# Kernel tuning notes

Measured on AMD Instinct MI355X. Metric: run time of the kernel, lower is better.

The kernel has to match this reference:

```python
import jax, jax.numpy as jnp
import numpy as np

ALPHA = 0.2      # LeakyReLU negative slope (alpha)
KNN = 5          # knn_num / cluster_num in get_center_1
M = 5            # m in get_dc
CC = 3           # cluster_centers
NEG = -9e15
EPS = 9e-15

def _pdist(x):
    sq = jnp.sum(x * x, axis=1)
    d2 = sq[:, None] + sq[None, :] - 2.0 * (x @ x.T)
    return jnp.sqrt(jnp.maximum(d2, 0.0))

def _cdist(x, c):
    d2 = jnp.sum(x * x, 1)[:, None] + jnp.sum(c * c, 1)[None, :] - 2.0 * (x @ c.T)
    return jnp.sqrt(jnp.maximum(d2, 0.0))

def _kmeans(x, k=CC, iters=10):
    # deterministic stand-in for sklearn KMeans(n_clusters=3, init='k-means++'):
    # farthest-point init + fixed Lloyd iterations
    c0 = x[0]
    d = jnp.sum((x - c0) ** 2, 1)
    c1 = x[jnp.argmax(d)]
    d = jnp.minimum(d, jnp.sum((x - c1) ** 2, 1))
    c2 = x[jnp.argmax(d)]
    centers = jnp.stack([c0, c1, c2])
    def step(c, _):
        assign = jnp.argmin(_cdist(x, c), axis=1)
        oh = jax.nn.one_hot(assign, k, dtype=x.dtype)
        newc = (oh.T @ x) / jnp.maximum(oh.sum(0), 1.0)[:, None]
        return newc, None
    centers, _ = jax.lax.scan(step, centers, None, length=iters)
    return centers

def _gravity(h):
    # get_center_1: fully built from detached tensors in the original -> stop_gradient
    x = jax.lax.stop_gradient(h)
    n = x.shape[0]
    z = _pdist(x)                                 # [n, n] pairwise distances
    negv, loc = jax.lax.top_k(-z, M + 1)          # M+1 smallest distances per row
    dc = jnp.mean(-negv[:, 1])                    # mean nearest-neighbor distance
    knn_idx = loc[:, 1:KNN + 1]                   # 5-NN (excluding self)
    rows = jnp.arange(n)[:, None]
    knn_vals = jnp.take_along_axis(z, knn_idx, axis=1)
    ori = jnp.zeros_like(z).at[rows, knn_idx].set(knn_vals)   # dists only at 5-NN
    nearest = jnp.take_along_axis(ori, loc[:, 1:2], axis=1)
    safe = jnp.where(ori != 0, ori, 1.0)
    ori = jnp.where(ori != 0, dc * nearest / (safe * safe), ori)
    # replicate the source's global flat-index mask (index = arange(size).reshape)
    flat = jnp.arange(n * n).reshape(n, n)
    mincol = jnp.min(jnp.argsort(ori, axis=1)[:, -KNN:], axis=1, keepdims=True)
    ori = jnp.where(flat >= mincol, 0.0, ori) - EPS
    centers = _kmeans(x)
    d1 = _cdist(x, centers)                       # [n, 3] node->center distances
    nearest1 = d1[:, 1:2]                         # cupy wrap: (i*3+1) % 3 == 1
    safe1 = jnp.where(d1 != 0, d1, 1.0)
    d1 = jnp.where(d1 != 0, dc * nearest1 / (safe1 * safe1), d1) - EPS
    z3 = jnp.full((CC, CC), NEG, dtype=x.dtype)
    top = jnp.concatenate([ori, d1], axis=1)
    bot = jnp.concatenate([d1.T, z3], axis=1)
    return jnp.concatenate([top, bot], axis=0)    # [(n+3), (n+3)]

def _forward(h, W, a, t1, t2):
    n, fin = h.shape
    fout = W.shape[1]
    Wh = h @ W
    s = Wh @ a[:fout] + (Wh @ a[fout:]).T         # [n, n]
    e = jnp.where(s > 0, s, ALPHA * s)            # LeakyReLU attention logits
    g = _gravity(h)
    att = jnp.concatenate([
        jnp.concatenate([e, t1], axis=1),
        jnp.concatenate([t2, jnp.zeros((CC, CC), h.dtype)], axis=1),
    ], axis=0)                                    # [(n+3), (n+3)]
    att = jax.nn.softmax(g @ att, axis=1)         # dropout omitted (eval mode)
    h_pad = jnp.concatenate([h, jnp.zeros((CC, fin), h.dtype)], axis=0)
    out = att @ (h_pad @ W)                       # [(n+3), fout]
    return jax.nn.elu(out)                        # concat=True

def setup_inputs():
    key = jax.random.key(0)
    k = jax.random.split(key, 5)
    N, FIN, FOUT = 4096, 512, 64
    gain = 1.414
    limW = gain * np.sqrt(6.0 / (FIN + FOUT))
    lima = gain * np.sqrt(6.0 / (2 * FOUT + 1))
    return {
        "h": jax.random.normal(k[0], (N, FIN), jnp.float32),
        "adj": jnp.zeros((N, N), jnp.float32),   # accepted but unused by forward
        "W": jax.random.uniform(k[1], (FIN, FOUT), jnp.float32, -limW, limW),
        "a": jax.random.uniform(k[2], (2 * FOUT, 1), jnp.float32, -lima, lima),
        "t1": jax.random.normal(k[3], (N, CC), jnp.float32),
        "t2": jax.random.normal(k[4], (CC, N), jnp.float32),
    }

def reference(h, adj, W, a, t1, t2):
    return _forward(h, W, a, t1, t2)
```

## Files before the change

kernel.cpp:

```cpp
#include <hip/hip_runtime.h>
#include <hip/hip_bf16.h>
#include <math.h>

#define NPTS 4096
#define FIN 512
#define FOUT 64
#define SCALE 4194304.0f
#define INVSCALE 2.384185791015625e-7f

typedef __attribute__((ext_vector_type(8))) short bf16x8;
typedef __attribute__((ext_vector_type(4))) float f32x4;
typedef unsigned long long ull;

static __device__ __forceinline__ unsigned short bfbits(float x) {
  __hip_bfloat16 b = __float2bfloat16(x);
  return *reinterpret_cast<unsigned short*>(&b);
}

static __device__ __forceinline__ float wsum64(float v) {
  #pragma unroll
  for (int mm = 1; mm < 64; mm <<= 1) v += __shfl_xor(v, mm);
  return v;
}

static __device__ __forceinline__ int aloadi(int* p) {
  return __hip_atomic_load(p, __ATOMIC_RELAXED, __HIP_MEMORY_SCOPE_AGENT);
}
static __device__ __forceinline__ ull aloadu(ull* p) {
  return __hip_atomic_load(p, __ATOMIC_RELAXED, __HIP_MEMORY_SCOPE_AGENT);
}

__global__ __launch_bounds__(256) void k_prep(const float* __restrict__ h,
    const float* __restrict__ W, __hip_bfloat16* __restrict__ xb,
    float* __restrict__ sq, int* __restrict__ m1, __hip_bfloat16* __restrict__ WbT,
    ull* __restrict__ accZ, int* __restrict__ cntZ, int* __restrict__ barZ) {
  int bid = blockIdx.x, t = threadIdx.x;
  if (bid >= 1026) {
    int idx = (bid - 1026) * 256 + t;
    #pragma unroll
    for (int s = 0; s < 10; ++s) accZ[s * 1536 + idx] = 0ull;
    if (idx < 40) cntZ[idx] = 0;
    if (idx < 16) barZ[idx] = 0;
    return;
  }
  if (bid >= 1024) {
    int base = (bid - 1024) * 16384;
    for (int rep = 0; rep < 64; ++rep) {
      int e = base + rep * 256 + t;
      int n = e >> 9, k = e & 511;
      WbT[e] = __float2bfloat16(W[k * FOUT + n]);
    }
    return;
  }
  int lane = t & 63, wid = t >> 6;
  int row = bid * 4 + wid;
  const float4* hr = (const float4*)(h + (size_t)row * FIN);
  float4 a = hr[lane], b = hr[64 + lane];
  ushort4 pa = { bfbits(a.x), bfbits(a.y), bfbits(a.z), bfbits(a.w) };
  ushort4 pb = { bfbits(b.x), bfbits(b.y), bfbits(b.z), bfbits(b.w) };
  *(ushort4*)(xb + (size_t)row * FIN + 4 * lane) = pa;
  *(ushort4*)(xb + (size_t)row * FIN + 256 + 4 * lane) = pb;
  float s = a.x*a.x + a.y*a.y + a.z*a.z + a.w*a.w
          + b.x*b.x + b.y*b.y + b.z*b.z + b.w*b.w;
  s = wsum64(s);
  if (lane == 0) { sq[row] = s; m1[row] = 0x7F800000; }
}

__device__ __forceinline__ void gram_role(const __hip_bfloat16* __restrict__ xb,
    const float* __restrict__ sq, int* __restrict__ m1, int gb, char* smem) {
  bool act = threadIdx.x < 256;
  int tid = threadIdx.x;
  int lane = tid & 63, wid = tid >> 6;
  int b = gb, I = 0;
  while (b >= 32 - I) { b -= 32 - I; ++I; }
  int J = I + b;
  char* As = smem;
  char* Bs = smem + 16384;

  int R0 = I * 128, C0 = J * 128;
  int rowBase = (wid >> 1) * 64;
  int colBase = (wid & 1) * 64;
  int lrow = lane & 15, hi = lane >> 4, rsub = hi * 4;

  f32x4 acc[4][4];
  #pragma unroll
  for (int p = 0; p < 4; ++p)
    #pragma unroll
    for (int q = 0; q < 4; ++q)
      acc[p][q] = (f32x4){0.f, 0.f, 0.f, 0.f};

  int srow = lane >> 3;
  int scol = ((lane & 7) ^ srow) * 8;
  const __hip_bfloat16* gA = xb + (size_t)(R0 + (wid & 3) * 32 + srow) * FIN + scol;
  const __hip_bfloat16* gB = xb + (size_t)(C0 + (wid & 3) * 32 + srow) * FIN + scol;
  char* lA = As + (wid & 3) * 4096;
  char* lB = Bs + (wid & 3) * 4096;
  int rdswz = (lrow & 7) << 4;

  for (int kt = 0; kt < 8; ++kt) {
    int K0 = kt * 64;
    if (act) {
      #pragma unroll
      for (int j = 0; j < 4; ++j) {
        __builtin_amdgcn_global_load_lds(
            (const __attribute__((address_space(1))) unsigned int*)(gA + (size_t)(8 * j) * FIN + K0),
            (__attribute__((address_space(3))) unsigned int*)(lA + j * 1024), 16, 0, 0);
        __builtin_amdgcn_global_load_lds(
            (const __attribute__((address_space(1))) unsigned int*)(gB + (size_t)(8 * j) * FIN + K0),
            (__attribute__((address_space(3))) unsigned int*)(lB + j * 1024), 16, 0, 0);
      }
    }
    __syncthreads();
    if (act) {
      #pragma unroll
      for (int s = 0; s < 2; ++s) {
        int k0b = s * 64;
        bf16x8 av[4], bw[4];
        #pragma unroll
        for (int f = 0; f < 4; ++f) {
          int arow = rowBase + f * 16 + lrow;
          av[f] = *(const bf16x8*)(As + arow * 128 + ((k0b + hi * 16) ^ rdswz));
          int brow = colBase + f * 16 + lrow;
          bw[f] = *(const bf16x8*)(Bs + brow * 128 + ((k0b + hi * 16) ^ rdswz));
        }
        #pragma unroll
        for (int fi = 0; fi < 4; ++fi)
          #pragma unroll
          for (int fj = 0; fj < 4; ++fj)
            acc[fi][fj] = __builtin_amdgcn_mfma_f32_16x16x32_bf16(av[fi], bw[fj], acc[fi][fj], 0, 0, 0);
      }
    }
    __syncthreads();
  }
  if (!act) return;

  int rowBaseG = R0 + rowBase, colBaseG = C0 + colBase;
  float sqr[16], sqc4[4];
  #pragma unroll
  for (int fi = 0; fi < 4; ++fi)
    #pragma unroll
    for (int rg = 0; rg < 4; ++rg)
      sqr[fi * 4 + rg] = sq[rowBaseG + fi * 16 + rsub + rg];
  #pragma unroll
  for (int fj = 0; fj < 4; ++fj) sqc4[fj] = sq[colBaseG + fj * 16 + lrow];

  float rmin[16], cmin[4];
  #pragma unroll
  for (int q = 0; q < 16; ++q) rmin[q] = INFINITY;
  #pragma unroll
  for (int q = 0; q < 4; ++q) cmin[q] = INFINITY;

  #pragma unroll
  for (int fi = 0; fi < 4; ++fi)
    #pragma unroll
    for (int fj = 0; fj < 4; ++fj)
      #pragma unroll
      for (int rg = 0; rg < 4; ++rg) {
        int r = rowBaseG + fi * 16 + rsub + rg;
        int c = colBaseG + fj * 16 + lrow;
        float d2 = sqr[fi * 4 + rg] + sqc4[fj] - 2.f * acc[fi][fj][rg];
        if (r == c) d2 = INFINITY;
        rmin[fi * 4 + rg] = fminf(rmin[fi * 4 + rg], d2);
        cmin[fj] = fminf(cmin[fj], d2);
      }

  #pragma unroll
  for (int mm = 1; mm < 16; mm <<= 1) {
    #pragma unroll
    for (int q = 0; q < 16; ++q) rmin[q] = fminf(rmin[q], __shfl_xor(rmin[q], mm));
  }
  if ((lane & 15) == 0) {
    #pragma unroll
    for (int q = 0; q < 16; ++q) {
      int r = rowBaseG + (q >> 2) * 16 + rsub + (q & 3);
      atomicMin(&m1[r], __float_as_int(rmin[q]));
    }
  }
  if (I != J) {
    #pragma unroll
    for (int mm = 16; mm < 64; mm <<= 1) {
      #pragma unroll
      for (int q = 0; q < 4; ++q) cmin[q] = fminf(cmin[q], __shfl_xor(cmin[q], mm));
    }
    if ((lane >> 4) == 0) {
      #pragma unroll
      for (int q = 0; q < 4; ++q)
        atomicMin(&m1[colBaseG + q * 16 + lane], __float_as_int(cmin[q]));
    }
  }
}

__device__ __forceinline__ void whmm_role(const __hip_bfloat16* __restrict__ xb,
    const __hip_bfloat16* __restrict__ WbT, float* __restrict__ Wh,
    __hip_bfloat16* __restrict__ WhbT, int wb) {
  int t = threadIdx.x, lane = t & 63, wid = t >> 6;
  int r16 = lane & 15, hi = lane >> 4;
  int rbase = wb * 128 + wid * 16;
  f32x4 acc[4];
  #pragma unroll
  for (int fn = 0; fn < 4; ++fn) acc[fn] = (f32x4){0.f, 0.f, 0.f, 0.f};
  const __hip_bfloat16* aP = xb + (size_t)(rbase + r16) * FIN + hi * 8;
  const __hip_bfloat16* bP[4];
  #pragma unroll
  for (int fn = 0; fn < 4; ++fn)
    bP[fn] = WbT + (size_t)(fn * 16 + r16) * FIN + hi * 8;
  #pragma unroll
  for (int kk = 0; kk < 16; ++kk) {
    bf16x8 a = *(const bf16x8*)(aP + kk * 32);
    #pragma unroll
    for (int fn = 0; fn < 4; ++fn) {
      bf16x8 bw = *(const bf16x8*)(bP[fn] + kk * 32);
      acc[fn] = __builtin_amdgcn_mfma_f32_16x16x32_bf16(a, bw, acc[fn], 0, 0, 0);
    }
  }
  #pragma unroll
  for (int fn = 0; fn < 4; ++fn)
    #pragma unroll
    for (int q = 0; q < 4; ++q) {
      float v = acc[fn][q];
      Wh[(size_t)(rbase + hi * 4 + q) * FOUT + fn * 16 + r16] = v;
      WhbT[(size_t)(fn * 16 + r16) * NPTS + rbase + hi * 4 + q] = __float2bfloat16(v);
    }
}

__device__ __forceinline__ void load_rows(const float* __restrict__ h, int rbase,
    int lane, float x[8][8]) {
  #pragma unroll
  for (int r = 0; r < 8; ++r) {
    const float4* xr = (const float4*)(h + (size_t)(rbase + r) * FIN);
    float4 u0 = xr[2 * lane], u1 = xr[2 * lane + 1];
    x[r][0]=u0.x; x[r][1]=u0.y; x[r][2]=u0.z; x[r][3]=u0.w;
    x[r][4]=u1.x; x[r][5]=u1.y; x[r][6]=u1.z; x[r][7]=u1.w;
  }
}

__device__ __forceinline__ void megabar(int* bar, int id) {
  __syncthreads();
  if (threadIdx.x == 0) {
    atomicAdd(&bar[id], 1);
    while (aloadi(&bar[id]) < 64) __builtin_amdgcn_s_sleep(2);
  }
  __syncthreads();
}

__global__ __launch_bounds__(512) void k_mega(
    const float* __restrict__ h, const float* __restrict__ sq,
    const __hip_bfloat16* __restrict__ xb, int* __restrict__ m1,
    const float* __restrict__ t2,
    int* __restrict__ bviA, int* __restrict__ biA,
    int* __restrict__ bviB, int* __restrict__ biB,
    float* __restrict__ tmpart, float* __restrict__ kvp, int* __restrict__ kip,
    ull* __restrict__ accum, int* __restrict__ cntAcc, int* __restrict__ bar,
    const __hip_bfloat16* __restrict__ WbT, float* __restrict__ Wh,
    __hip_bfloat16* __restrict__ WhbT) {
  __shared__ __align__(16) char smem[55552];
  int bid = blockIdx.x;
  if (bid >= 96) { gram_role(xb, sq, m1, bid - 96, smem); return; }
  if (bid >= 64) { whmm_role(xb, WbT, Wh, WhbT, bid - 64); return; }

  float* wsum  = (float*)smem;
  float* cents = (float*)(smem + 49152);
  float* rv    = (float*)(smem + 55296);
  int*   ri    = (int*)(smem + 55328);
  float* wcnt  = (float*)(smem + 55360);

  int t = threadIdx.x, lane = t & 63, wid = t >> 6, b = bid;
  int rbase = b * 64 + wid * 8;
  float x[8][8], sqr[8];
  load_rows(h, rbase, lane, x);
  #pragma unroll
  for (int r = 0; r < 8; ++r) sqr[r] = sq[rbase + r];

  float dloc[8];
  int b1, b2;

  {
    float cr[8];
    const float4* cp = (const float4*)h;
    float4 u0 = cp[2 * lane], u1 = cp[2 * lane + 1];
    cr[0]=u0.x;cr[1]=u0.y;cr[2]=u0.z;cr[3]=u0.w;cr[4]=u1.x;cr[5]=u1.y;cr[6]=u1.z;cr[7]=u1.w;
    float s0 = 0.f;
    #pragma unroll
    for (int q = 0; q < 8; ++q) s0 = fmaf(cr[q], cr[q], s0);
    float dd[8];
    #pragma unroll
    for (int r = 0; r < 8; ++r) dd[r] = 0.f;
    #pragma unroll
    for (int r = 0; r < 8; ++r)
      #pragma unroll
      for (int q = 0; q < 8; ++q) dd[r] = fmaf(x[r][q], cr[q], dd[r]);
    #pragma unroll
    for (int mm = 1; mm < 64; mm <<= 1) {
      s0 += __shfl_xor(s0, mm);
      #pragma unroll
      for (int r = 0; r < 8; ++r) dd[r] += __shfl_xor(dd[r], mm);
    }
    float bv = -1.f; int bi = 0;
    #pragma unroll
    for (int r = 0; r < 8; ++r) {
      float d = sqr[r] + s0 - 2.f * dd[r];
      dloc[r] = d;
      if (d > bv) { bv = d; bi = rbase + r; }
    }
    if (lane == 0) { rv[wid] = bv; ri[wid] = bi; }
  }
  __syncthreads();
  if (t == 0) {
    float vv = rv[0]; int ii = ri[0];
    for (int w = 1; w < 8; ++w)
      if (rv[w] > vv || (rv[w] == vv && ri[w] < ii)) { vv = rv[w]; ii = ri[w]; }
    int o1 = atomicExch(&bviA[b], __float_as_int(vv));
    int o2 = atomicExch(&biA[b], ii);
    asm volatile("" :: "v"(o1), "v"(o2));
    atomicAdd(&bar[0], 1);
  }
  if (wid == 1) {
    #pragma unroll
    for (int c = 0; c < 3; ++c) {
      float m = fabsf(t2[c * NPTS + b * 64 + lane]);
      #pragma unroll
      for (int mm = 1; mm < 64; mm <<= 1) m = fmaxf(m, __shfl_xor(m, mm));
      if (lane == 0) tmpart[b * 3 + c] = m;
    }
  } else if (wid == 2) {
    int k = b * 64 + lane;
    float v = t2[k] + t2[NPTS + k] + t2[2 * NPTS + k];
    int ki = k;
    #pragma unroll
    for (int mm = 1; mm < 64; mm <<= 1) {
      float ov = __shfl_xor(v, mm); int oi = __shfl_xor(ki, mm);
      if (ov < v || (ov == v && oi < ki)) { v = ov; ki = oi; }
    }
    if (lane == 0) { kvp[b] = v; kip[b] = ki; }
  }
  if (t == 0) { while (aloadi(&bar[0]) < 64) __builtin_amdgcn_s_sleep(2); }
  __syncthreads();
  {
    float v = __int_as_float(aloadi(&bviA[lane]));
    int i = aloadi(&biA[lane]);
    #pragma unroll
    for (int mm = 1; mm < 64; mm <<= 1) {
      float ov = __shfl_xor(v, mm); int oi = __shfl_xor(i, mm);
      if (ov > v || (ov == v && oi < i)) { v = ov; i = oi; }
    }
    b1 = i;
  }

  {
    float cr[8];
    const float4* cp = (const float4*)(h + (size_t)b1 * FIN);
    float4 u0 = cp[2 * lane], u1 = cp[2 * lane + 1];
    cr[0]=u0.x;cr[1]=u0.y;cr[2]=u0.z;cr[3]=u0.w;cr[4]=u1.x;cr[5]=u1.y;cr[6]=u1.z;cr[7]=u1.w;
    float s0 = 0.f;
    #pragma unroll
    for (int q = 0; q < 8; ++q) s0 = fmaf(cr[q], cr[q], s0);
    float dd[8];
    #pragma unroll
    for (int r = 0; r < 8; ++r) dd[r] = 0.f;
    #pragma unroll
    for (int r = 0; r < 8; ++r)
      #pragma unroll
      for (int q = 0; q < 8; ++q) dd[r] = fmaf(x[r][q], cr[q], dd[r]);
    #pragma unroll
    for (int mm = 1; mm < 64; mm <<= 1) {
      s0 += __shfl_xor(s0, mm);
      #pragma unroll
      for (int r = 0; r < 8; ++r) dd[r] += __shfl_xor(dd[r], mm);
    }
    float bv = -1.f; int bi = 0;
    #pragma unroll
    for (int r = 0; r < 8; ++r) {
      float d = fminf(sqr[r] + s0 - 2.f * dd[r], dloc[r]);
      dloc[r] = d;
      if (d > bv) { bv = d; bi = rbase + r; }
    }
    if (lane == 0) { rv[wid] = bv; ri[wid] = bi; }
  }
  __syncthreads();
  if (t == 0) {
    float vv = rv[0]; int ii = ri[0];
    for (int w = 1; w < 8; ++w)
      if (rv[w] > vv || (rv[w] == vv && ri[w] < ii)) { vv = rv[w]; ii = ri[w]; }
    int o1 = atomicExch(&bviB[b], __float_as_int(vv));
    int o2 = atomicExch(&biB[b], ii);
    asm volatile("" :: "v"(o1), "v"(o2));
    atomicAdd(&bar[1], 1);
    while (aloadi(&bar[1]) < 64) __builtin_amdgcn_s_sleep(2);
  }
  __syncthreads();
  {
    float v = __int_as_float(aloadi(&bviB[lane]));
    int i = aloadi(&biB[lane]);
    #pragma unroll
    for (int mm = 1; mm < 64; mm <<= 1) {
      float ov = __shfl_xor(v, mm); int oi = __shfl_xor(i, mm);
      if (ov > v || (ov == v && oi < i)) { v = ov; i = oi; }
    }
    b2 = i;
  }

  for (int it = 0; it < 10; ++it) {
    float c0r[8], c1r[8], c2r[8];
    if (it == 0) {
      const float4* p0 = (const float4*)h;
      const float4* p1 = (const float4*)(h + (size_t)b1 * FIN);
      const float4* p2 = (const float4*)(h + (size_t)b2 * FIN);
      float4 u;
      u = p0[2*lane];   c0r[0]=u.x;c0r[1]=u.y;c0r[2]=u.z;c0r[3]=u.w;
      u = p0[2*lane+1]; c0r[4]=u.x;c0r[5]=u.y;c0r[6]=u.z;c0r[7]=u.w;
      u = p1[2*lane];   c1r[0]=u.x;c1r[1]=u.y;c1r[2]=u.z;c1r[3]=u.w;
      u = p1[2*lane+1]; c1r[4]=u.x;c1r[5]=u.y;c1r[6]=u.z;c1r[7]=u.w;
      u = p2[2*lane];   c2r[0]=u.x;c2r[1]=u.y;c2r[2]=u.z;c2r[3]=u.w;
      u = p2[2*lane+1]; c2r[4]=u.x;c2r[5]=u.y;c2r[6]=u.z;c2r[7]=u.w;
    } else {
      ull* acc = accum + (size_t)(it - 1) * 1536;
      float cn[3];
      #pragma unroll
      for (int c = 0; c < 3; ++c)
        cn[c] = fmaxf((float)aloadi(&cntAcc[(it - 1) * 4 + c]), 1.f);
      for (int idx = t; idx < 1536; idx += 512)
        cents[idx] = (float)(long long)aloadu(&acc[idx]) * INVSCALE / cn[idx >> 9];
      __syncthreads();
      float4 u;
      u = *(const float4*)&cents[8*lane];        c0r[0]=u.x;c0r[1]=u.y;c0r[2]=u.z;c0r[3]=u.w;
      u = *(const float4*)&cents[8*lane+4];      c0r[4]=u.x;c0r[5]=u.y;c0r[6]=u.z;c0r[7]=u.w;
      u = *(const float4*)&cents[512+8*lane];    c1r[0]=u.x;c1r[1]=u.y;c1r[2]=u.z;c1r[3]=u.w;
      u = *(const float4*)&cents[512+8*lane+4];  c1r[4]=u.x;c1r[5]=u.y;c1r[6]=u.z;c1r[7]=u.w;
      u = *(const float4*)&cents[1024+8*lane];   c2r[0]=u.x;c2r[1]=u.y;c2r[2]=u.z;c2r[3]=u.w;
      u = *(const float4*)&cents[1024+8*lane+4]; c2r[4]=u.x;c2r[5]=u.y;c2r[6]=u.z;c2r[7]=u.w;
    }
    float s0 = 0.f, s1 = 0.f, s2 = 0.f;
    #pragma unroll
    for (int q = 0; q < 8; ++q) {
      s0 = fmaf(c0r[q], c0r[q], s0); s1 = fmaf(c1r[q], c1r[q], s1); s2 = fmaf(c2r[q], c2r[q], s2);
    }
    #pragma unroll
    for (int mm = 1; mm < 64; mm <<= 1) {
      s0 += __shfl_xor(s0, mm); s1 += __shfl_xor(s1, mm); s2 += __shfl_xor(s2, mm);
    }
    float d[8][3];
    #pragma unroll
    for (int r = 0; r < 8; ++r) { d[r][0] = 0.f; d[r][1] = 0.f; d[r][2] = 0.f; }
    #pragma unroll
    for (int r = 0; r < 8; ++r)
      #pragma unroll
      for (int q = 0; q < 8; ++q) {
        d[r][0] = fmaf(x[r][q], c0r[q], d[r][0]);
        d[r][1] = fmaf(x[r][q], c1r[q], d[r][1]);
        d[r][2] = fmaf(x[r][q], c2r[q], d[r][2]);
      }
    #pragma unroll
    for (int mm = 1; mm < 64; mm <<= 1) {
      #pragma unroll
      for (int r = 0; r < 8; ++r) {
        d[r][0] += __shfl_xor(d[r][0], mm);
        d[r][1] += __shfl_xor(d[r][1], mm);
        d[r][2] += __shfl_xor(d[r][2], mm);
      }
    }
    float ps[3][8];
    #pragma unroll
    for (int c = 0; c < 3; ++c)
      #pragma unroll
      for (int q = 0; q < 8; ++q) ps[c][q] = 0.f;
    float cnt0 = 0.f, cnt1 = 0.f, cnt2 = 0.f;
    #pragma unroll
    for (int r = 0; r < 8; ++r) {
      float e0 = sqr[r] + s0 - 2.f * d[r][0];
      float e1 = sqr[r] + s1 - 2.f * d[r][1];
      float e2 = sqr[r] + s2 - 2.f * d[r][2];
      int bc = 0; float bd = e0;
      if (e1 < bd) { bd = e1; bc = 1; }
      if (e2 < bd) { bd = e2; bc = 2; }
      float f0 = bc == 0 ? 1.f : 0.f, f1 = bc == 1 ? 1.f : 0.f, f2 = bc == 2 ? 1.f : 0.f;
      #pragma unroll
      for (int q = 0; q < 8; ++q) {
        ps[0][q] = fmaf(f0, x[r][q], ps[0][q]);
        ps[1][q] = fmaf(f1, x[r][q], ps[1][q]);
        ps[2][q] = fmaf(f2, x[r][q], ps[2][q]);
      }
      cnt0 += f0; cnt1 += f1; cnt2 += f2;
    }
    #pragma unroll
    for (int c = 0; c < 3; ++c) {
      *(float4*)&wsum[wid * 1536 + c * 512 + 8 * lane]     = make_float4(ps[c][0], ps[c][1], ps[c][2], ps[c][3]);
      *(float4*)&wsum[wid * 1536 + c * 512 + 8 * lane + 4] = make_float4(ps[c][4], ps[c][5], ps[c][6], ps[c][7]);
    }
    if (lane == 0) { wcnt[wid * 3 + 0] = cnt0; wcnt[wid * 3 + 1] = cnt1; wcnt[wid * 3 + 2] = cnt2; }
    __syncthreads();
    ull* accO = accum + (size_t)it * 1536;
    for (int idx = t; idx < 1536; idx += 512) {
      float s = ((wsum[0*1536+idx] + wsum[1*1536+idx]) + (wsum[2*1536+idx] + wsum[3*1536+idx]))
              + ((wsum[4*1536+idx] + wsum[5*1536+idx]) + (wsum[6*1536+idx] + wsum[7*1536+idx]));
      long long q = llrintf(s * SCALE);
      ull old = atomicAdd(&accO[idx], (ull)q);
      asm volatile("" :: "v"(old));
    }
    if (t < 3) {
      float s = 0.f;
      for (int w = 0; w < 8; ++w) s += wcnt[w * 3 + t];
      int old = atomicAdd(&cntAcc[it * 4 + t], (int)(s + 0.5f));
      asm volatile("" :: "v"(old));
    }
    if (it < 9) megabar(bar, 2 + it);
  }
}

__global__ __launch_bounds__(512) void k_mainC(
    const float* __restrict__ h, const float* __restrict__ sq,
    const float* __restrict__ t2, const __hip_bfloat16* __restrict__ WhbT,
    const float* __restrict__ Wh, const int* __restrict__ m1,
    const ull* __restrict__ accIn, const int* __restrict__ cntIn,
    const float* __restrict__ tmpart, const float* __restrict__ kvp,
    const int* __restrict__ kip, float* __restrict__ out) {
  __shared__ float t2s[3 * 4096];
  __shared__ float VcS[8][16][68];
  __shared__ float SpS[8][16];
  __shared__ float Mrow[16];
  __shared__ float a012[16][3];
  __shared__ float cents[1536];
  __shared__ float cntS[3];
  __shared__ float tmS[3];
  __shared__ float red[8];
  __shared__ int skstar;
  int t = threadIdx.x, lane = t & 63, wid = t >> 6;
  int R0 = blockIdx.x * 16;
  for (int idx = t; idx < 3072; idx += 512)
    ((f32x4*)t2s)[idx] = ((const f32x4*)t2)[idx];
  if (t < 3) {
    cntS[t] = fmaxf((float)cntIn[t], 1.f);
    float m = 0.f;
    for (int q = 0; q < 64; ++q) m = fmaxf(m, tmpart[q * 3 + t]);
    tmS[t] = m;
  }
  float sdc = 0.f;
  #pragma unroll
  for (int q = 0; q < 8; ++q)
    sdc += sqrtf(fmaxf(__int_as_float(m1[t + 512 * q]), 0.f));
  sdc = wsum64(sdc);
  if (lane == 0) red[wid] = sdc;
  __syncthreads();
  for (int idx = t; idx < 1536; idx += 512)
    cents[idx] = (float)(long long)accIn[idx] * INVSCALE / cntS[idx >> 9];
  __syncthreads();
  float dcv = (((red[0] + red[1]) + (red[2] + red[3])) + ((red[4] + red[5]) + (red[6] + red[7])))
            * (1.f / (float)NPTS);
  {
    float c0r[8], c1r[8], c2r[8];
    float4 u;
    u = *(const float4*)&cents[8 * lane];          c0r[0]=u.x;c0r[1]=u.y;c0r[2]=u.z;c0r[3]=u.w;
    u = *(const float4*)&cents[8 * lane + 4];      c0r[4]=u.x;c0r[5]=u.y;c0r[6]=u.z;c0r[7]=u.w;
    u = *(const float4*)&cents[512 + 8 * lane];    c1r[0]=u.x;c1r[1]=u.y;c1r[2]=u.z;c1r[3]=u.w;
    u = *(const float4*)&cents[512 + 8 * lane + 4];c1r[4]=u.x;c1r[5]=u.y;c1r[6]=u.z;c1r[7]=u.w;
    u = *(const float4*)&cents[1024 + 8 * lane];   c2r[0]=u.x;c2r[1]=u.y;c2r[2]=u.z;c2r[3]=u.w;
    u = *(const float4*)&cents[1024 + 8*lane + 4]; c2r[4]=u.x;c2r[5]=u.y;c2r[6]=u.z;c2r[7]=u.w;
    float s0 = 0.f, s1 = 0.f, s2 = 0.f;
    #pragma unroll
    for (int q = 0; q < 8; ++q) {
      s0 = fmaf(c0r[q], c0r[q], s0); s1 = fmaf(c1r[q], c1r[q], s1); s2 = fmaf(c2r[q], c2r[q], s2);
    }
    float xr2[2][8];
    #pragma unroll
    for (int rr = 0; rr < 2; ++rr) {
      int row = R0 + 2 * wid + rr;
      const float4* xr = (const float4*)(h + (size_t)row * FIN);
      float4 u0 = xr[2 * lane], u1 = xr[2 * lane + 1];
      xr2[rr][0]=u0.x; xr2[rr][1]=u0.y; xr2[rr][2]=u0.z; xr2[rr][3]=u0.w;
      xr2[rr][4]=u1.x; xr2[rr][5]=u1.y; xr2[rr][6]=u1.z; xr2[rr][7]=u1.w;
    }
    float dd[2][3];
    #pragma unroll
    for (int rr = 0; rr < 2; ++rr) { dd[rr][0]=0.f; dd[rr][1]=0.f; dd[rr][2]=0.f; }
    #pragma unroll
    for (int rr = 0; rr < 2; ++rr)
      #pragma unroll
      for (int q = 0; q < 8; ++q) {
        dd[rr][0] = fmaf(xr2[rr][q], c0r[q], dd[rr][0]);
        dd[rr][1] = fmaf(xr2[rr][q], c1r[q], dd[rr][1]);
        dd[rr][2] = fmaf(xr2[rr][q], c2r[q], dd[rr][2]);
      }
    #pragma unroll
    for (int mm = 1; mm < 64; mm <<= 1) {
      s0 += __shfl_xor(s0, mm); s1 += __shfl_xor(s1, mm); s2 += __shfl_xor(s2, mm);
      #pragma unroll
      for (int rr = 0; rr < 2; ++rr) {
        dd[rr][0] += __shfl_xor(dd[rr][0], mm);
        dd[rr][1] += __shfl_xor(dd[rr][1], mm);
        dd[rr][2] += __shfl_xor(dd[rr][2], mm);
      }
    }
    if (lane == 0) {
      #pragma unroll
      for (int rr = 0; rr < 2; ++rr) {
        int row = R0 + 2 * wid + rr;
        float sr = sq[row];
        float q0 = sqrtf(fmaxf(sr + s0 - 2.f * dd[rr][0], 0.f));
        float q1 = sqrtf(fmaxf(sr + s1 - 2.f * dd[rr][1], 0.f));
        float q2 = sqrtf(fmaxf(sr + s2 - 2.f * dd[rr][2], 0.f));
        float nr = q1;
        float a0 = (q0 != 0.f) ? (dcv * nr / (q0 * q0)) : 0.f;
        float a1 = (q1 != 0.f) ? (dcv * nr / (q1 * q1)) : 0.f;
        float a2 = (q2 != 0.f) ? (dcv * nr / (q2 * q2)) : 0.f;
        a012[2 * wid + rr][0] = a0; a012[2 * wid + rr][1] = a1; a012[2 * wid + rr][2] = a2;
        Mrow[2 * wid + rr] = fmaf(fabsf(a2), tmS[2], fmaf(fabsf(a1), tmS[1], fabsf(a0) * tmS[0]));
      }
    }
  }
  __syncthreads();
  int r16 = lane & 15, hi = lane >> 4;
  float a0 = a012[r16][0], a1 = a012[r16][1], a2 = a012[r16][2];
  float M = Mrow[r16];
  int K0 = wid * 512;
  f32x4 acc[4];
  #pragma unroll
  for (int fn = 0; fn < 4; ++fn) acc[fn] = (f32x4){0.f, 0.f, 0.f, 0.f};
  float Sp = 0.f;
  const __hip_bfloat16* bwB[4];
  #pragma unroll
  for (int fn = 0; fn < 4; ++fn)
    bwB[fn] = WhbT + (size_t)(fn * 16 + r16) * NPTS + K0 + hi * 8;

  for (int kst = 0; kst < 16; ++kst) {
    int kb = K0 + kst * 32 + hi * 8;
    f32x4 c0a = *(const f32x4*)&t2s[kb],        c0b = *(const f32x4*)&t2s[kb + 4];
    f32x4 c1a = *(const f32x4*)&t2s[4096 + kb], c1b = *(const f32x4*)&t2s[4096 + kb + 4];
    f32x4 c2a = *(const f32x4*)&t2s[8192 + kb], c2b = *(const f32x4*)&t2s[8192 + kb + 4];
    float pv[8];
    #pragma unroll
    for (int j = 0; j < 4; ++j) {
      float L  = fmaf(a0, c0a[j], fmaf(a1, c1a[j], fmaf(a2, c2a[j], -M)));
      pv[j] = __expf(L);
      float L2 = fmaf(a0, c0b[j], fmaf(a1, c1b[j], fmaf(a2, c2b[j], -M)));
      pv[4 + j] = __expf(L2);
    }
    Sp += ((pv[0] + pv[1]) + (pv[2] + pv[3])) + ((pv[4] + pv[5]) + (pv[6] + pv[7]));
    union { bf16x8 v; __hip_bfloat162 h2[4]; } pa;
    #pragma unroll
    for (int jj = 0; jj < 4; ++jj) {
      float2 f2; f2.x = pv[2 * jj]; f2.y = pv[2 * jj + 1];
      pa.h2[jj] = __float22bfloat162_rn(f2);
    }
    #pragma unroll
    for (int fn = 0; fn < 4; ++fn) {
      bf16x8 bw = *(const bf16x8*)(bwB[fn] + kst * 32);
      acc[fn] = __builtin_amdgcn_mfma_f32_16x16x32_bf16(pa.v, bw, acc[fn], 0, 0, 0);
    }
  }
  Sp += __shfl_xor(Sp, 16);
  Sp += __shfl_xor(Sp, 32);
  if (hi == 0) SpS[wid][r16] = Sp;
  #pragma unroll
  for (int fn = 0; fn < 4; ++fn)
    #pragma unroll
    for (int q = 0; q < 4; ++q)
      VcS[wid][hi * 4 + q][fn * 16 + r16] = acc[fn][q];
  __syncthreads();
  for (int e = t; e < 1024; e += 512) {
    int row = e >> 6, col = e & 63;
    float V = 0.f;
    #pragma unroll
    for (int w = 0; w < 8; ++w) V += VcS[w][row][col];
    float S = 3.f * __expf(-Mrow[row]);
    #pragma unroll
    for (int w = 0; w < 8; ++w) S += SpS[w][row];
    float o = V / S;
    out[(size_t)(R0 + row) * FOUT + col] = o > 0.f ? o : expm1f(o);
  }
  if (blockIdx.x == 0) {
    if (wid == 0) {
      float v = kvp[lane]; int i = kip[lane];
      #pragma unroll
      for (int mm = 1; mm < 64; mm <<= 1) {
        float ov = __shfl_xor(v, mm); int oi = __shfl_xor(i, mm);
        if (ov < v || (ov == v && oi < i)) { v = ov; i = oi; }
      }
      if (lane == 0) skstar = i;
    }
    __syncthreads();
    int kstar = skstar;
    if (t < 192) {
      int c = t >> 6, j = t & 63;
      float wv = Wh[(size_t)kstar * FOUT + j];
      out[(size_t)(NPTS + c) * FOUT + j] = wv > 0.f ? wv : expm1f(wv);
    }
  }
}

extern "C" void kernel_launch(void* const* d_in, const int* in_sizes, int n_in,
                              void* d_out, int out_size, void* d_ws, size_t ws_size,
                              hipStream_t stream) {
  const float* h  = (const float*)d_in[0];
  const float* W  = (const float*)d_in[2];
  const float* t2 = (const float*)d_in[5];
  float* out = (float*)d_out;

  char* ws = (char*)d_ws;
  __hip_bfloat16* xb = (__hip_bfloat16*)ws;
  float* F = (float*)(ws + (size_t)NPTS * FIN * 2);
  float* sq   = F + 0;
  int*   m1   = (int*)(F + 4096);
  float* Wh   = F + 32768;
  __hip_bfloat16* WhbT = (__hip_bfloat16*)(F + 1756672);
  __hip_bfloat16* WbT  = (__hip_bfloat16*)(F + 1887744);
  float* G = F + 1904128;
  int*   bviA   = (int*)(G + 0);
  int*   biA    = (int*)(G + 64);
  int*   bviB   = (int*)(G + 128);
  int*   biB    = (int*)(G + 192);
  float* tmpart = G + 384;
  float* kvp    = G + 576;
  int*   kip    = (int*)(G + 640);
  int*   bar    = (int*)(G + 704);
  ull*   accum  = (ull*)(G + 768);
  int*   cntAcc = (int*)(G + 768 + 30720);

  k_prep<<<1032, 256, 0, stream>>>(h, W, xb, sq, m1, WbT, accum, cntAcc, bar);
  k_mega<<<624, 512, 0, stream>>>(h, sq, xb, m1, t2, bviA, biA, bviB, biB,
                                  tmpart, kvp, kip, accum, cntAcc, bar, WbT, Wh, WhbT);
  k_mainC<<<256, 512, 0, stream>>>(h, sq, t2, WhbT, Wh, m1,
                                   (const ull*)(accum + 9 * 1536), (const int*)(cntAcc + 9 * 4),
                                   tmpart, kvp, kip, out);
}
```

Measured before the change: 162.0 us.

## Replace fixed-point atomic centroid accumulation with per-block partials and distributed reduction

The k-means centroid update previously had every block atomically add scaled 64-bit fixed-point partial sums into one global accumulator per iteration. That accumulator had to be zeroed in a prep kernel and re-read by every block. Now each block writes its partial sums into a transposed per-block slot. After a grid barrier, each block reduces a 24-element slice across the 64 blocks and writes the final centroids, and a second barrier publishes them. This removes contended atomics and the zeroing pass, at the cost of doubling the number of grid-wide barriers per iteration.

```diff
diff --git a/kernel.cpp b/kernel.cpp
--- a/kernel.cpp
+++ b/kernel.cpp
@@ -5,12 +5,9 @@
 #define NPTS 4096
 #define FIN 512
 #define FOUT 64
-#define SCALE 4194304.0f
-#define INVSCALE 2.384185791015625e-7f
 
 typedef __attribute__((ext_vector_type(8))) short bf16x8;
 typedef __attribute__((ext_vector_type(4))) float f32x4;
-typedef unsigned long long ull;
 
 static __device__ __forceinline__ unsigned short bfbits(float x) {
   __hip_bfloat16 b = __float2bfloat16(x);
@@ -26,21 +23,21 @@
 static __device__ __forceinline__ int aloadi(int* p) {
   return __hip_atomic_load(p, __ATOMIC_RELAXED, __HIP_MEMORY_SCOPE_AGENT);
 }
-static __device__ __forceinline__ ull aloadu(ull* p) {
+static __device__ __forceinline__ float aloadf(float* p) {
   return __hip_atomic_load(p, __ATOMIC_RELAXED, __HIP_MEMORY_SCOPE_AGENT);
+}
+static __device__ __forceinline__ void axchf(float* p, float v) {
+  float old = atomicExch(p, v);
+  asm volatile("" :: "v"(old));
 }
 
 __global__ __launch_bounds__(256) void k_prep(const float* __restrict__ h,
     const float* __restrict__ W, __hip_bfloat16* __restrict__ xb,
     float* __restrict__ sq, int* __restrict__ m1, __hip_bfloat16* __restrict__ WbT,
-    ull* __restrict__ accZ, int* __restrict__ cntZ, int* __restrict__ barZ) {
+    int* __restrict__ barZ) {
   int bid = blockIdx.x, t = threadIdx.x;
   if (bid >= 1026) {
-    int idx = (bid - 1026) * 256 + t;
-    #pragma unroll
-    for (int s = 0; s < 10; ++s) accZ[s * 1536 + idx] = 0ull;
-    if (idx < 40) cntZ[idx] = 0;
-    if (idx < 16) barZ[idx] = 0;
+    if (t < 32) barZ[t] = 0;
     return;
   }
   if (bid >= 1024) {
@@ -250,7 +247,8 @@
     int* __restrict__ bviA, int* __restrict__ biA,
     int* __restrict__ bviB, int* __restrict__ biB,
     float* __restrict__ tmpart, float* __restrict__ kvp, int* __restrict__ kip,
-    ull* __restrict__ accum, int* __restrict__ cntAcc, int* __restrict__ bar,
+    float* __restrict__ psT, float* __restrict__ pcT, float* __restrict__ centsG,
+    int* __restrict__ bar,
     const __hip_bfloat16* __restrict__ WbT, float* __restrict__ Wh,
     __hip_bfloat16* __restrict__ WhbT) {
   __shared__ __align__(16) char smem[55552];
@@ -263,6 +261,7 @@
   float* rv    = (float*)(smem + 55296);
   int*   ri    = (int*)(smem + 55328);
   float* wcnt  = (float*)(smem + 55360);
+  float* cntB  = (float*)(smem + 55456);
 
   int t = threadIdx.x, lane = t & 63, wid = t >> 6, b = bid;
   int rbase = b * 64 + wid * 8;
@@ -413,14 +412,6 @@
       u = p2[2*lane];   c2r[0]=u.x;c2r[1]=u.y;c2r[2]=u.z;c2r[3]=u.w;
       u = p2[2*lane+1]; c2r[4]=u.x;c2r[5]=u.y;c2r[6]=u.z;c2r[7]=u.w;
     } else {
-      ull* acc = accum + (size_t)(it - 1) * 1536;
-      float cn[3];
-      #pragma unroll
-      for (int c = 0; c < 3; ++c)
-        cn[c] = fmaxf((float)aloadi(&cntAcc[(it - 1) * 4 + c]), 1.f);
-      for (int idx = t; idx < 1536; idx += 512)
-        cents[idx] = (float)(long long)aloadu(&acc[idx]) * INVSCALE / cn[idx >> 9];
-      __syncthreads();
       float4 u;
       u = *(const float4*)&cents[8*lane];        c0r[0]=u.x;c0r[1]=u.y;c0r[2]=u.z;c0r[3]=u.w;
       u = *(const float4*)&cents[8*lane+4];      c0r[4]=u.x;c0r[5]=u.y;c0r[6]=u.z;c0r[7]=u.w;
@@ -488,21 +479,44 @@
     }
     if (lane == 0) { wcnt[wid * 3 + 0] = cnt0; wcnt[wid * 3 + 1] = cnt1; wcnt[wid * 3 + 2] = cnt2; }
     __syncthreads();
-    ull* accO = accum + (size_t)it * 1536;
-    for (int idx = t; idx < 1536; idx += 512) {
-      float s = ((wsum[0*1536+idx] + wsum[1*1536+idx]) + (wsum[2*1536+idx] + wsum[3*1536+idx]))
-              + ((wsum[4*1536+idx] + wsum[5*1536+idx]) + (wsum[6*1536+idx] + wsum[7*1536+idx]));
-      long long q = llrintf(s * SCALE);
-      ull old = atomicAdd(&accO[idx], (ull)q);
-      asm volatile("" :: "v"(old));
+    #pragma unroll
+    for (int j = 0; j < 3; ++j) {
+      int e = t + j * 512;
+      float s = ((wsum[0*1536+e] + wsum[1*1536+e]) + (wsum[2*1536+e] + wsum[3*1536+e]))
+              + ((wsum[4*1536+e] + wsum[5*1536+e]) + (wsum[6*1536+e] + wsum[7*1536+e]));
+      axchf(&psT[(size_t)e * 64 + b], s);
     }
     if (t < 3) {
       float s = 0.f;
       for (int w = 0; w < 8; ++w) s += wcnt[w * 3 + t];
-      int old = atomicAdd(&cntAcc[it * 4 + t], (int)(s + 0.5f));
-      asm volatile("" :: "v"(old));
-    }
-    if (it < 9) megabar(bar, 2 + it);
+      axchf(&pcT[t * 64 + b], s);
+    }
+    megabar(bar, 2 + 2 * it);
+    if (wid < 3) {
+      float v = aloadf(&pcT[wid * 64 + lane]);
+      v = wsum64(v);
+      if (lane == 0) cntB[wid] = fmaxf(v, 1.f);
+    }
+    float rsum[3];
+    #pragma unroll
+    for (int j = 0; j < 3; ++j) {
+      int e = 24 * b + wid * 3 + j;
+      float v = aloadf(&psT[(size_t)e * 64 + lane]);
+      rsum[j] = wsum64(v);
+    }
+    __syncthreads();
+    if (lane == 0) {
+      #pragma unroll
+      for (int j = 0; j < 3; ++j) {
+        int e = 24 * b + wid * 3 + j;
+        axchf(&centsG[e], rsum[j] / cntB[e >> 9]);
+      }
+    }
+    if (it < 9) {
+      megabar(bar, 3 + 2 * it);
+      for (int idx = t; idx < 1536; idx += 512) cents[idx] = aloadf(&centsG[idx]);
+      __syncthreads();
+    }
   }
 }
 
@@ -510,7 +524,7 @@
     const float* __restrict__ h, const float* __restrict__ sq,
     const float* __restrict__ t2, const __hip_bfloat16* __restrict__ WhbT,
     const float* __restrict__ Wh, const int* __restrict__ m1,
-    const ull* __restrict__ accIn, const int* __restrict__ cntIn,
+    const float* __restrict__ centsG,
     const float* __restrict__ tmpart, const float* __restrict__ kvp,
     const int* __restrict__ kip, float* __restrict__ out) {
   __shared__ float t2s[3 * 4096];
@@ -519,7 +533,6 @@
   __shared__ float Mrow[16];
   __shared__ float a012[16][3];
   __shared__ float cents[1536];
-  __shared__ float cntS[3];
   __shared__ float tmS[3];
   __shared__ float red[8];
   __shared__ int skstar;
@@ -528,7 +541,6 @@
   for (int idx = t; idx < 3072; idx += 512)
     ((f32x4*)t2s)[idx] = ((const f32x4*)t2)[idx];
   if (t < 3) {
-    cntS[t] = fmaxf((float)cntIn[t], 1.f);
     float m = 0.f;
     for (int q = 0; q < 64; ++q) m = fmaxf(m, tmpart[q * 3 + t]);
     tmS[t] = m;
@@ -539,9 +551,7 @@
     sdc += sqrtf(fmaxf(__int_as_float(m1[t + 512 * q]), 0.f));
   sdc = wsum64(sdc);
   if (lane == 0) red[wid] = sdc;
-  __syncthreads();
-  for (int idx = t; idx < 1536; idx += 512)
-    cents[idx] = (float)(long long)accIn[idx] * INVSCALE / cntS[idx >> 9];
+  for (int idx = t; idx < 1536; idx += 512) cents[idx] = centsG[idx];
   __syncthreads();
   float dcv = (((red[0] + red[1]) + (red[2] + red[3])) + ((red[4] + red[5]) + (red[6] + red[7])))
             * (1.f / (float)NPTS);
@@ -711,13 +721,13 @@
   float* kvp    = G + 576;
   int*   kip    = (int*)(G + 640);
   int*   bar    = (int*)(G + 704);
-  ull*   accum  = (ull*)(G + 768);
-  int*   cntAcc = (int*)(G + 768 + 30720);
-
-  k_prep<<<1032, 256, 0, stream>>>(h, W, xb, sq, m1, WbT, accum, cntAcc, bar);
+  float* centsG = G + 768;
+  float* pcT    = G + 2304;
+  float* psT    = G + 2560;
+
+  k_prep<<<1027, 256, 0, stream>>>(h, W, xb, sq, m1, WbT, bar);
   k_mega<<<624, 512, 0, stream>>>(h, sq, xb, m1, t2, bviA, biA, bviB, biB,
-                                  tmpart, kvp, kip, accum, cntAcc, bar, WbT, Wh, WhbT);
-  k_mainC<<<256, 512, 0, stream>>>(h, sq, t2, WhbT, Wh, m1,
-                                   (const ull*)(accum + 9 * 1536), (const int*)(cntAcc + 9 * 4),
+                                  tmpart, kvp, kip, psT, pcT, centsG, bar, WbT, Wh, WhbT);
+  k_mainC<<<256, 512, 0, stream>>>(h, sq, t2, WhbT, Wh, m1, centsG,
                                    tmpart, kvp, kip, out);
 }
```

Result: slower. 216.0 us (+33.4%).
